# Performance work log

Hardware: AMD Instinct MI355X
Metric: run time of the kernel (lower is better)

The kernel has to match this reference:

```python
import jax, jax.numpy as jnp
import numpy as np

N = 262144          # num_nodes
H = 512             # hidden_dim
NH = 8              # num_heads
HD = H // NH        # head_dim = 64
C = 32              # num_centroids
MOM = 0.99          # centroid EMA momentum
LN_EPS = 1e-5


def setup_inputs() -> dict:
    key = jax.random.key(0)
    ks = jax.random.split(key, 12)
    s = 0.02
    return {
        "x": jax.random.normal(ks[0], (N, H), dtype=jnp.float32),
        "centroids": jax.random.normal(ks[1], (C, H), dtype=jnp.float32),
        "Wq": jax.random.normal(ks[2], (H, H), dtype=jnp.float32) * s,
        "bq": jnp.zeros((H,), jnp.float32),
        "Wk": jax.random.normal(ks[3], (H, H), dtype=jnp.float32) * s,
        "bk": jnp.zeros((H,), jnp.float32),
        "Wv": jax.random.normal(ks[4], (H, H), dtype=jnp.float32) * s,
        "bv": jnp.zeros((H,), jnp.float32),
        "Wo": jax.random.normal(ks[5], (H, H), dtype=jnp.float32) * s,
        "bo": jnp.zeros((H,), jnp.float32),
        "ln_w": jnp.ones((H,), jnp.float32),
        "ln_b": jnp.zeros((H,), jnp.float32),
    }


def _update_centroids(x, centroids):
    # nearest-centroid assignment (argmin of squared euclidean == argmin of cdist)
    d2 = (
        jnp.sum(x * x, axis=1, keepdims=True)
        - 2.0 * (x @ centroids.T)
        + jnp.sum(centroids * centroids, axis=1)[None, :]
    )  # [N, C]
    assign = jnp.argmin(d2, axis=1)  # [N]
    sums = jax.ops.segment_sum(x, assign, num_segments=C)           # [C, H]
    counts = jax.ops.segment_sum(jnp.ones((x.shape[0],), x.dtype), assign, num_segments=C)  # [C]
    means = sums / jnp.maximum(counts, 1.0)[:, None]
    updated = jnp.where(
        (counts > 0)[:, None], MOM * centroids + (1.0 - MOM) * means, centroids
    )
    # torch update is in no_grad; value changes but grads flow to the param identity-style
    return centroids + jax.lax.stop_gradient(updated - centroids)


def reference(x, centroids, Wq, bq, Wk, bk, Wv, bv, Wo, bo, ln_w, ln_b):
    residual = x
    centroids = _update_centroids(x, centroids)  # training-mode EMA k-means step

    q = (x @ Wq + bq).reshape(-1, NH, HD)           # [N, nh, hd]
    k = (centroids @ Wk + bk).reshape(C, NH, HD)    # [C, nh, hd]
    v = (centroids @ Wv + bv).reshape(C, NH, HD)

    scores = jnp.einsum("nhd,chd->nhc", q, k) / np.sqrt(HD).astype(np.float32)
    attn = jax.nn.softmax(scores, axis=-1)          # dropout = identity (eval semantics)
    ctx = jnp.einsum("nhc,chd->nhd", attn, v).reshape(-1, H)

    out = ctx @ Wo + bo
    y = out + residual
    mu = jnp.mean(y, axis=-1, keepdims=True)
    var = jnp.mean((y - mu) ** 2, axis=-1, keepdims=True)
    return (y - mu) * jax.lax.rsqrt(var + LN_EPS) * ln_w + ln_b
```

## Files before the change

kernel.cpp:

```cpp
#include <hip/hip_runtime.h>

#define NN 262144
#define HH 512
#define CC 32
#define MOMF 0.99f

#define WS_SUMS   0
#define WS_COUNTS 131072
#define WS_UPD    131328
#define WS_KBUF   147712
#define WS_VBUF   164096
#define WS_SB     180480
#define WS_MT     180736
#define WS_PT     246272
#define WS_ASSIGN 279040

typedef __attribute__((ext_vector_type(8))) short s8v;
typedef __attribute__((ext_vector_type(4))) float f4v;
typedef __attribute__((ext_vector_type(4))) unsigned int u4v;

static __device__ __forceinline__ unsigned short f2bf(float f) {
  unsigned int u = __float_as_uint(f);
  u += 0x7FFFu + ((u >> 16) & 1u);
  return (unsigned short)(u >> 16);
}
static __device__ __forceinline__ unsigned int pk2bf(float a, float b) {
  return (unsigned int)f2bf(a) | ((unsigned int)f2bf(b) << 16);
}
#define EL4(v, k) ((k) == 0 ? (v).x : (k) == 1 ? (v).y : (k) == 2 ? (v).z : (v).w)

__global__ __launch_bounds__(256) void k_asn(const float* __restrict__ x,
                                             const float* __restrict__ cent,
                                             unsigned char* __restrict__ sag) {
  __shared__ __align__(16) unsigned char smem[34432];
  unsigned short* clbf = (unsigned short*)smem;
  float* cnS = (float*)(smem + 33280);
  float* scratch = (float*)(smem + 33408);

  const int tid = threadIdx.x;
  const int w = tid >> 6, l = tid & 63;
  const int l16 = l & 15, g = l >> 4;

  for (int i = tid * 8; i < CC * HH; i += 256 * 8) {
    float4 a = *(const float4*)&cent[i];
    float4 b = *(const float4*)&cent[i + 4];
    const int row = i >> 9, col = i & 511;
    u4v p;
    p[0] = pk2bf(a.x, a.y); p[1] = pk2bf(a.z, a.w);
    p[2] = pk2bf(b.x, b.y); p[3] = pk2bf(b.z, b.w);
    *(u4v*)((unsigned char*)clbf + row * 1040 + col * 2) = p;
  }
  {
    const int c = tid >> 3, kk = tid & 7;
    float p = 0.f;
    for (int m = 0; m < 64; ++m) { float v = cent[c * HH + kk + 8 * m]; p += v * v; }
    scratch[tid] = p;
  }
  __syncthreads();
  if (tid < CC) {
    float s = 0.f;
#pragma unroll
    for (int m = 0; m < 8; ++m) s += scratch[tid * 8 + m];
    cnS[tid] = s;
  }
  __syncthreads();

  float cnr[8];
#pragma unroll
  for (int tc = 0; tc < 2; ++tc)
#pragma unroll
    for (int r = 0; r < 4; ++r) cnr[tc * 4 + r] = cnS[tc * 16 + 4 * g + r];

  for (int pass = 0; pass < 2; ++pass) {
    const int nodeloc = pass * 64 + w * 16 + l16;
    const float* xr = x + ((size_t)blockIdx.x * 128 + nodeloc) * HH;
    f4v acc[2];
    acc[0] = (f4v){0.f, 0.f, 0.f, 0.f};
    acc[1] = (f4v){0.f, 0.f, 0.f, 0.f};
    float4 pa[2][4], pb[2][4];
#pragma unroll
    for (int k = 0; k < 4; ++k) {
      pa[0][k] = *(const float4*)&xr[k * 32 + g * 8];
      pb[0][k] = *(const float4*)&xr[k * 32 + g * 8 + 4];
    }
#pragma unroll
    for (int c4 = 0; c4 < 4; ++c4) {
      const int cur = c4 & 1, nxt = cur ^ 1;
      if (c4 < 3) {
#pragma unroll
        for (int k = 0; k < 4; ++k) {
          const int kk = (c4 + 1) * 4 + k;
          pa[nxt][k] = *(const float4*)&xr[kk * 32 + g * 8];
          pb[nxt][k] = *(const float4*)&xr[kk * 32 + g * 8 + 4];
        }
      }
#pragma unroll
      for (int k = 0; k < 4; ++k) {
        const int kk = c4 * 4 + k;
        float4 xa = pa[cur][k], xb = pb[cur][k];
        s8v bfrag;
        bfrag[0] = (short)f2bf(xa.x); bfrag[1] = (short)f2bf(xa.y);
        bfrag[2] = (short)f2bf(xa.z); bfrag[3] = (short)f2bf(xa.w);
        bfrag[4] = (short)f2bf(xb.x); bfrag[5] = (short)f2bf(xb.y);
        bfrag[6] = (short)f2bf(xb.z); bfrag[7] = (short)f2bf(xb.w);
#pragma unroll
        for (int tc = 0; tc < 2; ++tc) {
          s8v afrag = *(const s8v*)((unsigned char*)clbf +
                                    (tc * 16 + l16) * 1040 + kk * 64 + g * 16);
          acc[tc] = __builtin_amdgcn_mfma_f32_16x16x32_bf16(afrag, bfrag, acc[tc], 0, 0, 0);
        }
      }
    }
    float bv = 3.4e38f; int bi = 0;
#pragma unroll
    for (int tc = 0; tc < 2; ++tc)
#pragma unroll
      for (int r = 0; r < 4; ++r) {
        const int c = tc * 16 + 4 * g + r;
        const float v = cnr[tc * 4 + r] - 2.f * acc[tc][r];
        if (v < bv) { bv = v; bi = c; }
      }
#pragma unroll
    for (int m = 16; m <= 32; m <<= 1) {
      const float ov = __shfl_xor(bv, m);
      const int oi = __shfl_xor(bi, m);
      if (ov < bv || (ov == bv && oi < bi)) { bv = ov; bi = oi; }
    }
    if (l < 16) sag[(size_t)blockIdx.x * 128 + nodeloc] = (unsigned char)bi;
  }
}

__global__ __launch_bounds__(256) void k_sum(const float* __restrict__ x,
                                             const unsigned char* __restrict__ sag,
                                             float* __restrict__ gsums,
                                             float* __restrict__ gcounts) {
  __shared__ __align__(16) unsigned char xt[32768];
  const int tid = threadIdx.x;
  const int w = tid >> 6, l = tid & 63;
  const int l16 = l & 15, g = l >> 4;
  const int q = tid & 7, cc = tid >> 3;
  const size_t node0 = (size_t)blockIdx.x * 512;
  const unsigned char* sab = sag + node0;

  f4v acc[8][2];
#pragma unroll
  for (int ct = 0; ct < 8; ++ct) {
    acc[ct][0] = (f4v){0.f, 0.f, 0.f, 0.f};
    acc[ct][1] = (f4v){0.f, 0.f, 0.f, 0.f};
  }

  for (int step = 0; step < 16; ++step) {
    float4 r[4][4];
    const float* xs = x + (node0 + step * 32 + q * 4) * HH + cc * 16;
#pragma unroll
    for (int nn = 0; nn < 4; ++nn)
#pragma unroll
      for (int f = 0; f < 4; ++f)
        r[nn][f] = *(const float4*)&xs[nn * HH + f * 4];
    const uint2 awv = *(const uint2*)(sab + step * 32 + 8 * g);
    __syncthreads();
#pragma unroll
    for (int j = 0; j < 16; ++j) {
      uint2 p;
      p.x = pk2bf(EL4(r[0][j >> 2], j & 3), EL4(r[1][j >> 2], j & 3));
      p.y = pk2bf(EL4(r[2][j >> 2], j & 3), EL4(r[3][j >> 2], j & 3));
      *(uint2*)(xt + (cc * 16 + j) * 64 + q * 8) = p;
    }
    __syncthreads();
    s8v oh0, oh1;
#pragma unroll
    for (int j = 0; j < 8; ++j) {
      const unsigned a = ((j < 4 ? awv.x >> (8 * j) : awv.y >> (8 * (j - 4)))) & 255u;
      oh0[j] = (a == (unsigned)l16) ? (short)0x3F80 : (short)0;
      oh1[j] = (a == (unsigned)(16 + l16)) ? (short)0x3F80 : (short)0;
    }
#pragma unroll
    for (int ct = 0; ct < 8; ++ct) {
      s8v af = *(const s8v*)(xt + (w * 128 + ct * 16 + l16) * 64 + g * 16);
      acc[ct][0] = __builtin_amdgcn_mfma_f32_16x16x32_bf16(af, oh0, acc[ct][0], 0, 0, 0);
      acc[ct][1] = __builtin_amdgcn_mfma_f32_16x16x32_bf16(af, oh1, acc[ct][1], 0, 0, 0);
    }
  }

  const int pb = blockIdx.x & 7;
#pragma unroll
  for (int ct = 0; ct < 8; ++ct)
#pragma unroll
    for (int tc = 0; tc < 2; ++tc) {
      const int c = tc * 16 + l16;
      const int xcol = w * 128 + ct * 16 + 4 * g;
#pragma unroll
      for (int r = 0; r < 4; ++r)
        atomicAdd(&gsums[pb * 16384 + c * HH + xcol + r], acc[ct][tc][r]);
    }

  if (w == 0 && l < CC) {
    int cnt = 0;
    for (int i = 0; i < 512; i += 4) {
      const unsigned wd = *(const unsigned*)(sab + i);
      cnt += (int)((wd & 255u) == (unsigned)l) + (int)(((wd >> 8) & 255u) == (unsigned)l) +
             (int)(((wd >> 16) & 255u) == (unsigned)l) + (int)(((wd >> 24) & 255u) == (unsigned)l);
    }
    atomicAdd(&gcounts[pb * 32 + l], (float)cnt);
  }
}

__global__ void k_upd(const float* __restrict__ cent, const float* __restrict__ sums,
                      const float* __restrict__ counts, float* __restrict__ upd) {
  const int i = blockIdx.x * 256 + threadIdx.x;
  const int c = i >> 9;
  float s = 0.f, cnt = 0.f;
#pragma unroll
  for (int b = 0; b < 8; ++b) { s += sums[b * 16384 + i]; cnt += counts[b * 32 + c]; }
  const float mean = s / fmaxf(cnt, 1.f);
  upd[i] = (cnt > 0.f) ? (MOMF * cent[i] + (1.f - MOMF) * mean) : cent[i];
}

__global__ void k_kv(const float* __restrict__ upd,
                     const float* __restrict__ Wk, const float* __restrict__ bk,
                     const float* __restrict__ Wv, const float* __restrict__ bv,
                     float* __restrict__ kbuf, float* __restrict__ vbuf) {
  const int o = blockIdx.x * 256 + threadIdx.x;
  const int sel = o >> 14;
  const int idx = o & 16383;
  const int c = idx >> 9, j = idx & 511;
  const float* W = sel ? Wv : Wk;
  const float* b = sel ? bv : bk;
  const float* u = upd + c * HH;
  float s = b[j];
  for (int i = 0; i < HH; ++i) s += u[i] * W[i * HH + j];
  (sel ? vbuf : kbuf)[idx] = s;
}

__global__ void k_msp(const float* __restrict__ Wq, const float* __restrict__ bq,
                      const float* __restrict__ kbuf, const float* __restrict__ vbuf,
                      const float* __restrict__ Wo, const float* __restrict__ bo,
                      unsigned short* __restrict__ Mt, float* __restrict__ sb,
                      unsigned short* __restrict__ Pt) {
  const int b = blockIdx.x, t = threadIdx.x;
  const float scale = 0.125f;
  if (b < 512) {
    const int o = b * 256 + t;
    const int hc = o >> 9, i = o & 511;
    const int h = hc >> 5, c = hc & 31;
    const float* wq = Wq + i * HH + h * 64;
    const float* kr = kbuf + c * HH + h * 64;
    float s = 0.f;
#pragma unroll
    for (int d = 0; d < 64; ++d) s += wq[d] * kr[d];
    Mt[(i >> 5) * 8192 + hc * 32 + (i & 31)] = f2bf(s * scale);
  } else if (b < 1024) {
    const int o = b - 512;
    const int hc = t;
    const int h = hc >> 5, c = hc & 31;
    const float* vr = vbuf + c * HH + h * 64;
    const float* wo = Wo + h * 64 * HH + o;
    float s = 0.f;
#pragma unroll
    for (int d = 0; d < 64; ++d) s += vr[d] * wo[d * HH];
    Pt[h * 16384 + o * 32 + (hc & 31)] = f2bf(s + bo[o] * scale);
  } else if (t < 256) {
    const int h = t >> 5, c = t & 31;
    const float* kr = kbuf + c * HH + h * 64;
    const float* bqp = bq + h * 64;
    float s = 0.f;
#pragma unroll
    for (int d = 0; d < 64; ++d) s += bqp[d] * kr[d];
    sb[t] = s * scale;
  }
}

__global__ __launch_bounds__(256, 2) void k_main(
    const float* __restrict__ x, const unsigned short* __restrict__ Mt,
    const float* __restrict__ sb, const unsigned short* __restrict__ Pt,
    const float* __restrict__ lnw, const float* __restrict__ lnb,
    float* __restrict__ y) {
  __shared__ __align__(16) unsigned char smem[40960];
  float* yb = (float*)smem;
  const unsigned char* Mtb = (const unsigned char*)Mt;
  const unsigned char* Ptb = (const unsigned char*)Pt;
  const int tid = threadIdx.x;
  const int w = tid >> 6, l = tid & 63;
  const int l16 = l & 15, g = l >> 4;
  const size_t n0 = (size_t)blockIdx.x * 64;
  const size_t xrow = n0 + w * 16 + l16;
  const float* xr = x + xrow * HH;

  f4v acc1[16];
#pragma unroll
  for (int tc = 0; tc < 16; ++tc)
    acc1[tc] = *(const f4v*)&sb[tc * 16 + 4 * g];

  for (int kk = 0; kk < 16; ++kk) {
    float4 xa = *(const float4*)&xr[kk * 32 + g * 8];
    float4 xb = *(const float4*)&xr[kk * 32 + g * 8 + 4];
    __syncthreads();
#pragma unroll
    for (int r = 0; r < 4; ++r)
      *(u4v*)(smem + tid * 80 + r * 16) =
          *(const u4v*)(Mtb + kk * 16384 + tid * 64 + r * 16);
    __syncthreads();
    s8v bfrag;
    bfrag[0] = (short)f2bf(xa.x); bfrag[1] = (short)f2bf(xa.y);
    bfrag[2] = (short)f2bf(xa.z); bfrag[3] = (short)f2bf(xa.w);
    bfrag[4] = (short)f2bf(xb.x); bfrag[5] = (short)f2bf(xb.y);
    bfrag[6] = (short)f2bf(xb.z); bfrag[7] = (short)f2bf(xb.w);
#pragma unroll
    for (int tc = 0; tc < 16; ++tc) {
      s8v afrag = *(const s8v*)(smem + (tc * 16 + l16) * 80 + g * 16);
      acc1[tc] = __builtin_amdgcn_mfma_f32_16x16x32_bf16(afrag, bfrag, acc1[tc], 0, 0, 0);
    }
  }

  unsigned int apk[16][2];
#pragma unroll
  for (int h = 0; h < 8; ++h) {
    f4v s0 = acc1[2 * h], s1 = acc1[2 * h + 1];
    float m = fmaxf(fmaxf(fmaxf(s0[0], s0[1]), fmaxf(s0[2], s0[3])),
                    fmaxf(fmaxf(s1[0], s1[1]), fmaxf(s1[2], s1[3])));
    m = fmaxf(m, __shfl_xor(m, 16));
    m = fmaxf(m, __shfl_xor(m, 32));
    float e0 = __expf(s0[0] - m), e1 = __expf(s0[1] - m);
    float e2 = __expf(s0[2] - m), e3 = __expf(s0[3] - m);
    float e4 = __expf(s1[0] - m), e5 = __expf(s1[1] - m);
    float e6 = __expf(s1[2] - m), e7 = __expf(s1[3] - m);
    float sum = ((e0 + e1) + (e2 + e3)) + ((e4 + e5) + (e6 + e7));
    sum += __shfl_xor(sum, 16);
    sum += __shfl_xor(sum, 32);
    const float inv = 1.f / sum;
    apk[2 * h][0] = pk2bf(e0 * inv, e1 * inv);
    apk[2 * h][1] = pk2bf(e2 * inv, e3 * inv);
    apk[2 * h + 1][0] = pk2bf(e4 * inv, e5 * inv);
    apk[2 * h + 1][1] = pk2bf(e6 * inv, e7 * inv);
  }

  f4v acc2[32];
#pragma unroll
  for (int to = 0; to < 32; ++to) acc2[to] = (f4v){0.f, 0.f, 0.f, 0.f};

  for (int h = 0; h < 8; ++h) {
    unsigned int dw[4];
#pragma unroll
    for (int d = 0; d < 4; ++d) {
      const int gsrc = 2 * (g & 1) + (d >> 1);
      const int src = l16 + 16 * gsrc;
      unsigned int t0 = (unsigned int)__shfl((int)apk[2 * h][d & 1], src, 64);
      unsigned int t1 = (unsigned int)__shfl((int)apk[2 * h + 1][d & 1], src, 64);
      dw[d] = (g < 2) ? t0 : t1;
    }
    u4v bu; bu[0] = dw[0]; bu[1] = dw[1]; bu[2] = dw[2]; bu[3] = dw[3];
    s8v bfrag = __builtin_bit_cast(s8v, bu);
    __syncthreads();
#pragma unroll
    for (int oo = 0; oo < 2; ++oo)
#pragma unroll
      for (int q = 0; q < 4; ++q)
        *(u4v*)(smem + (tid + 256 * oo) * 80 + q * 16) =
            *(const u4v*)(Ptb + h * 32768 + (tid + 256 * oo) * 64 + q * 16);
    __syncthreads();
#pragma unroll
    for (int to = 0; to < 32; ++to) {
      s8v afrag = *(const s8v*)(smem + (to * 16 + l16) * 80 + g * 16);
      acc2[to] = __builtin_amdgcn_mfma_f32_16x16x32_bf16(afrag, bfrag, acc2[to], 0, 0, 0);
    }
  }

  float s1 = 0.f, s2 = 0.f;
#pragma unroll
  for (int to = 0; to < 32; ++to) {
    float4 xv = *(const float4*)&xr[to * 16 + 4 * g];
    acc2[to][0] += xv.x; acc2[to][1] += xv.y;
    acc2[to][2] += xv.z; acc2[to][3] += xv.w;
    s1 += (acc2[to][0] + acc2[to][1]) + (acc2[to][2] + acc2[to][3]);
    s2 += (acc2[to][0] * acc2[to][0] + acc2[to][1] * acc2[to][1]) +
          (acc2[to][2] * acc2[to][2] + acc2[to][3] * acc2[to][3]);
  }
  s1 += __shfl_xor(s1, 16); s2 += __shfl_xor(s2, 16);
  s1 += __shfl_xor(s1, 32); s2 += __shfl_xor(s2, 32);
  const float mean = s1 * (1.f / 512.f);
  const float var = s2 * (1.f / 512.f) - mean * mean;
  const float rstd = rsqrtf(var + 1e-5f);
#pragma unroll
  for (int to = 0; to < 32; ++to) {
    float4 wv = *(const float4*)&lnw[to * 16 + 4 * g];
    float4 bv = *(const float4*)&lnb[to * 16 + 4 * g];
    acc2[to][0] = (acc2[to][0] - mean) * rstd * wv.x + bv.x;
    acc2[to][1] = (acc2[to][1] - mean) * rstd * wv.y + bv.y;
    acc2[to][2] = (acc2[to][2] - mean) * rstd * wv.z + bv.z;
    acc2[to][3] = (acc2[to][3] - mean) * rstd * wv.w + bv.w;
  }

  const int prow = tid >> 7;
  const int pc = (tid & 127) * 4;
  for (int j = 0; j < 4; ++j) {
    __syncthreads();
    if (w == j) {
#pragma unroll
      for (int to = 0; to < 32; ++to)
        *(f4v*)&yb[l16 * 520 + to * 16 + 4 * g] = acc2[to];
    }
    __syncthreads();
#pragma unroll
    for (int p = 0; p < 8; ++p)
      *(float4*)&y[(n0 + j * 16 + p * 2 + prow) * HH + pc] =
          *(const float4*)&yb[(p * 2 + prow) * 520 + pc];
  }
}

extern "C" void kernel_launch(void* const* d_in, const int* in_sizes, int n_in,
                              void* d_out, int out_size, void* d_ws, size_t ws_size,
                              hipStream_t stream) {
  const float* x    = (const float*)d_in[0];
  const float* cent = (const float*)d_in[1];
  const float* Wq   = (const float*)d_in[2];
  const float* bq   = (const float*)d_in[3];
  const float* Wk   = (const float*)d_in[4];
  const float* bk   = (const float*)d_in[5];
  const float* Wv   = (const float*)d_in[6];
  const float* bv   = (const float*)d_in[7];
  const float* Wo   = (const float*)d_in[8];
  const float* bo   = (const float*)d_in[9];
  const float* lnw  = (const float*)d_in[10];
  const float* lnb  = (const float*)d_in[11];
  float* ws = (float*)d_ws;
  float* y  = (float*)d_out;

  hipMemsetAsync(ws, 0, (8 * 16384 + 8 * 32) * sizeof(float), stream);
  k_asn<<<2048, 256, 0, stream>>>(x, cent, (unsigned char*)(ws + WS_ASSIGN));
  k_sum<<<512, 256, 0, stream>>>(x, (const unsigned char*)(ws + WS_ASSIGN),
                                 ws + WS_SUMS, ws + WS_COUNTS);
  k_upd<<<64, 256, 0, stream>>>(cent, ws + WS_SUMS, ws + WS_COUNTS, ws + WS_UPD);
  k_kv<<<128, 256, 0, stream>>>(ws + WS_UPD, Wk, bk, Wv, bv,
                                ws + WS_KBUF, ws + WS_VBUF);
  k_msp<<<1025, 256, 0, stream>>>(Wq, bq, ws + WS_KBUF, ws + WS_VBUF, Wo, bo,
                                  (unsigned short*)(ws + WS_MT), ws + WS_SB,
                                  (unsigned short*)(ws + WS_PT));
  k_main<<<4096, 256, 0, stream>>>(x, (const unsigned short*)(ws + WS_MT),
                                   ws + WS_SB, (const unsigned short*)(ws + WS_PT),
                                   lnw, lnb, y);
}
```

Before: 880.9 us.

## Double-buffer weight tiles in LDS with register prefetch across both GEMM phases

Both MFMA loops in k_main now use two 20 KB LDS buffers. The next weight tile and the next x chunk are loaded into registers before the current tile's MFMAs run, then written to the other buffer, so each step needs one barrier instead of two. The second GEMM is split into 16 half-head steps so each step's tile fits a buffer, and the last step of the first GEMM prefetches the first P tile. The aim is to hide global-load latency behind MFMA work and cut synchronisation, at the cost of more registers, which may hurt occupancy under launch_bounds(256,2).

```diff
diff --git a/kernel.cpp b/kernel.cpp
--- a/kernel.cpp
+++ b/kernel.cpp
@@ -286,30 +286,55 @@
   const size_t xrow = n0 + w * 16 + l16;
   const float* xr = x + xrow * HH;
 
+  {
+    const unsigned char* src = Mtb + tid * 64;
+    u4v r0 = *(const u4v*)(src), r1 = *(const u4v*)(src + 16);
+    u4v r2 = *(const u4v*)(src + 32), r3 = *(const u4v*)(src + 48);
+    unsigned char* dst = smem + tid * 80;
+    *(u4v*)(dst) = r0; *(u4v*)(dst + 16) = r1;
+    *(u4v*)(dst + 32) = r2; *(u4v*)(dst + 48) = r3;
+  }
+  float4 xa_c = *(const float4*)&xr[g * 8];
+  float4 xb_c = *(const float4*)&xr[g * 8 + 4];
+  __syncthreads();
+
   f4v acc1[16];
 #pragma unroll
   for (int tc = 0; tc < 16; ++tc)
     acc1[tc] = *(const f4v*)&sb[tc * 16 + 4 * g];
 
+#pragma unroll
   for (int kk = 0; kk < 16; ++kk) {
-    float4 xa = *(const float4*)&xr[kk * 32 + g * 8];
-    float4 xb = *(const float4*)&xr[kk * 32 + g * 8 + 4];
-    __syncthreads();
-#pragma unroll
-    for (int r = 0; r < 4; ++r)
-      *(u4v*)(smem + tid * 80 + r * 16) =
-          *(const u4v*)(Mtb + kk * 16384 + tid * 64 + r * 16);
-    __syncthreads();
+    const int cur = (kk & 1) * 20480, nxt = ((kk + 1) & 1) * 20480;
+    u4v r0, r1, r2, r3;
+    float4 xa_n, xb_n;
+    {
+      const unsigned char* src =
+          (kk < 15) ? (Mtb + (kk + 1) * 16384 + tid * 64) : (Ptb + tid * 64);
+      r0 = *(const u4v*)(src); r1 = *(const u4v*)(src + 16);
+      r2 = *(const u4v*)(src + 32); r3 = *(const u4v*)(src + 48);
+    }
+    if (kk < 15) {
+      xa_n = *(const float4*)&xr[(kk + 1) * 32 + g * 8];
+      xb_n = *(const float4*)&xr[(kk + 1) * 32 + g * 8 + 4];
+    }
     s8v bfrag;
-    bfrag[0] = (short)f2bf(xa.x); bfrag[1] = (short)f2bf(xa.y);
-    bfrag[2] = (short)f2bf(xa.z); bfrag[3] = (short)f2bf(xa.w);
-    bfrag[4] = (short)f2bf(xb.x); bfrag[5] = (short)f2bf(xb.y);
-    bfrag[6] = (short)f2bf(xb.z); bfrag[7] = (short)f2bf(xb.w);
+    bfrag[0] = (short)f2bf(xa_c.x); bfrag[1] = (short)f2bf(xa_c.y);
+    bfrag[2] = (short)f2bf(xa_c.z); bfrag[3] = (short)f2bf(xa_c.w);
+    bfrag[4] = (short)f2bf(xb_c.x); bfrag[5] = (short)f2bf(xb_c.y);
+    bfrag[6] = (short)f2bf(xb_c.z); bfrag[7] = (short)f2bf(xb_c.w);
 #pragma unroll
     for (int tc = 0; tc < 16; ++tc) {
-      s8v afrag = *(const s8v*)(smem + (tc * 16 + l16) * 80 + g * 16);
+      s8v afrag = *(const s8v*)(smem + cur + (tc * 16 + l16) * 80 + g * 16);
       acc1[tc] = __builtin_amdgcn_mfma_f32_16x16x32_bf16(afrag, bfrag, acc1[tc], 0, 0, 0);
     }
+    {
+      unsigned char* dst = smem + nxt + tid * 80;
+      *(u4v*)(dst) = r0; *(u4v*)(dst + 16) = r1;
+      *(u4v*)(dst + 32) = r2; *(u4v*)(dst + 48) = r3;
+    }
+    __syncthreads();
+    if (kk < 15) { xa_c = xa_n; xb_c = xb_n; }
   }
 
   unsigned int apk[16][2];
@@ -338,7 +363,16 @@
 #pragma unroll
   for (int to = 0; to < 32; ++to) acc2[to] = (f4v){0.f, 0.f, 0.f, 0.f};
 
-  for (int h = 0; h < 8; ++h) {
+#pragma unroll
+  for (int s = 0; s < 16; ++s) {
+    const int cur = (s & 1) * 20480, nxt = ((s + 1) & 1) * 20480;
+    const int h = s >> 1, half = s & 1;
+    u4v r0, r1, r2, r3;
+    if (s < 15) {
+      const unsigned char* src = Ptb + (s + 1) * 16384 + tid * 64;
+      r0 = *(const u4v*)(src); r1 = *(const u4v*)(src + 16);
+      r2 = *(const u4v*)(src + 32); r3 = *(const u4v*)(src + 48);
+    }
     unsigned int dw[4];
 #pragma unroll
     for (int d = 0; d < 4; ++d) {
@@ -350,19 +384,18 @@
     }
     u4v bu; bu[0] = dw[0]; bu[1] = dw[1]; bu[2] = dw[2]; bu[3] = dw[3];
     s8v bfrag = __builtin_bit_cast(s8v, bu);
-    __syncthreads();
-#pragma unroll
-    for (int oo = 0; oo < 2; ++oo)
-#pragma unroll
-      for (int q = 0; q < 4; ++q)
-        *(u4v*)(smem + (tid + 256 * oo) * 80 + q * 16) =
-            *(const u4v*)(Ptb + h * 32768 + (tid + 256 * oo) * 64 + q * 16);
-    __syncthreads();
-#pragma unroll
-    for (int to = 0; to < 32; ++to) {
-      s8v afrag = *(const s8v*)(smem + (to * 16 + l16) * 80 + g * 16);
-      acc2[to] = __builtin_amdgcn_mfma_f32_16x16x32_bf16(afrag, bfrag, acc2[to], 0, 0, 0);
-    }
+#pragma unroll
+    for (int tl = 0; tl < 16; ++tl) {
+      s8v afrag = *(const s8v*)(smem + cur + (tl * 16 + l16) * 80 + g * 16);
+      acc2[half * 16 + tl] =
+          __builtin_amdgcn_mfma_f32_16x16x32_bf16(afrag, bfrag, acc2[half * 16 + tl], 0, 0, 0);
+    }
+    if (s < 15) {
+      unsigned char* dst = smem + nxt + tid * 80;
+      *(u4v*)(dst) = r0; *(u4v*)(dst + 16) = r1;
+      *(u4v*)(dst + 32) = r2; *(u4v*)(dst + 48) = r3;
+    }
+    __syncthreads();
   }
 
   float s1 = 0.f, s2 = 0.f;
```

Result: no change. 877.9 us (-0.3%).

## Load MFMA weight fragments directly from global memory instead of LDS staging

Applied to the files above, without the earlier changes.

Removes the per-iteration LDS staging of the Mt and Pt weight tiles along with their __syncthreads barriers. Each lane now reads its A fragment straight from global memory (expected to hit L2/L1 since the weights are small and shared by all blocks). The loops are fully unrolled and the second GEMM is split into 16 half-steps. This drops barrier stalls and LDS traffic, but adds many global loads per wave and more register pressure from the full unroll.

```diff
diff --git a/kernel.cpp b/kernel.cpp
--- a/kernel.cpp
+++ b/kernel.cpp
@@ -275,8 +275,7 @@
     const float* __restrict__ sb, const unsigned short* __restrict__ Pt,
     const float* __restrict__ lnw, const float* __restrict__ lnb,
     float* __restrict__ y) {
-  __shared__ __align__(16) unsigned char smem[40960];
-  float* yb = (float*)smem;
+  __shared__ __align__(16) float yb[16 * 520];
   const unsigned char* Mtb = (const unsigned char*)Mt;
   const unsigned char* Ptb = (const unsigned char*)Pt;
   const int tid = threadIdx.x;
@@ -285,29 +284,26 @@
   const size_t n0 = (size_t)blockIdx.x * 64;
   const size_t xrow = n0 + w * 16 + l16;
   const float* xr = x + xrow * HH;
+  const int laneoff = l16 * 64 + g * 16;
 
   f4v acc1[16];
 #pragma unroll
   for (int tc = 0; tc < 16; ++tc)
     acc1[tc] = *(const f4v*)&sb[tc * 16 + 4 * g];
 
+#pragma unroll
   for (int kk = 0; kk < 16; ++kk) {
     float4 xa = *(const float4*)&xr[kk * 32 + g * 8];
     float4 xb = *(const float4*)&xr[kk * 32 + g * 8 + 4];
-    __syncthreads();
-#pragma unroll
-    for (int r = 0; r < 4; ++r)
-      *(u4v*)(smem + tid * 80 + r * 16) =
-          *(const u4v*)(Mtb + kk * 16384 + tid * 64 + r * 16);
-    __syncthreads();
     s8v bfrag;
     bfrag[0] = (short)f2bf(xa.x); bfrag[1] = (short)f2bf(xa.y);
     bfrag[2] = (short)f2bf(xa.z); bfrag[3] = (short)f2bf(xa.w);
     bfrag[4] = (short)f2bf(xb.x); bfrag[5] = (short)f2bf(xb.y);
     bfrag[6] = (short)f2bf(xb.z); bfrag[7] = (short)f2bf(xb.w);
+    const unsigned char* base = Mtb + kk * 16384 + laneoff;
 #pragma unroll
     for (int tc = 0; tc < 16; ++tc) {
-      s8v afrag = *(const s8v*)(smem + (tc * 16 + l16) * 80 + g * 16);
+      s8v afrag = *(const s8v*)(base + tc * 1024);
       acc1[tc] = __builtin_amdgcn_mfma_f32_16x16x32_bf16(afrag, bfrag, acc1[tc], 0, 0, 0);
     }
   }
@@ -338,7 +334,9 @@
 #pragma unroll
   for (int to = 0; to < 32; ++to) acc2[to] = (f4v){0.f, 0.f, 0.f, 0.f};
 
-  for (int h = 0; h < 8; ++h) {
+#pragma unroll
+  for (int s = 0; s < 16; ++s) {
+    const int h = s >> 1, half = s & 1;
     unsigned int dw[4];
 #pragma unroll
     for (int d = 0; d < 4; ++d) {
@@ -350,18 +348,12 @@
     }
     u4v bu; bu[0] = dw[0]; bu[1] = dw[1]; bu[2] = dw[2]; bu[3] = dw[3];
     s8v bfrag = __builtin_bit_cast(s8v, bu);
-    __syncthreads();
-#pragma unroll
-    for (int oo = 0; oo < 2; ++oo)
-#pragma unroll
-      for (int q = 0; q < 4; ++q)
-        *(u4v*)(smem + (tid + 256 * oo) * 80 + q * 16) =
-            *(const u4v*)(Ptb + h * 32768 + (tid + 256 * oo) * 64 + q * 16);
-    __syncthreads();
-#pragma unroll
-    for (int to = 0; to < 32; ++to) {
-      s8v afrag = *(const s8v*)(smem + (to * 16 + l16) * 80 + g * 16);
-      acc2[to] = __builtin_amdgcn_mfma_f32_16x16x32_bf16(afrag, bfrag, acc2[to], 0, 0, 0);
+    const unsigned char* base = Ptb + s * 16384 + laneoff;
+#pragma unroll
+    for (int tl = 0; tl < 16; ++tl) {
+      s8v afrag = *(const s8v*)(base + tl * 1024);
+      acc2[half * 16 + tl] =
+          __builtin_amdgcn_mfma_f32_16x16x32_bf16(afrag, bfrag, acc2[half * 16 + tl], 0, 0, 0);
     }
   }
 
```

After: 1.052 ms. 19.4% more time.
